# Kernel optimization log

Measured on AMD Instinct MI355X. Metric: run time of the kernel, lower is better.

The kernel has to match this reference:

```python
import jax, jax.numpy as jnp
import numpy as np

B, S, E, H = 4, 1024, 512, 8
DK = E // H


def setup_inputs() -> dict:
    key = jax.random.key(0)
    ks = jax.random.split(key, 16)
    s = 1.0 / np.sqrt(E)
    inp = {
        "query": jax.random.normal(ks[0], (B, S, E), dtype=jnp.float32),
        "key": jax.random.normal(ks[1], (B, S, E), dtype=jnp.float32),
        "value": jax.random.normal(ks[2], (B, S, E), dtype=jnp.float32),
        "dist_conv": jax.random.uniform(ks[3], (B, S, S), dtype=jnp.float32),
        "mask": jax.random.randint(ks[4], (B, S, S), 0, 2, dtype=jnp.int32),
        # four Linear(E, E) layers: q, k, v, out (torch: y = x @ W.T + b)
        "Wq": jax.random.normal(ks[5], (E, E), dtype=jnp.float32) * s,
        "bq": jnp.zeros((E,), dtype=jnp.float32),
        "Wk": jax.random.normal(ks[6], (E, E), dtype=jnp.float32) * s,
        "bk": jnp.zeros((E,), dtype=jnp.float32),
        "Wv": jax.random.normal(ks[7], (E, E), dtype=jnp.float32) * s,
        "bv": jnp.zeros((E,), dtype=jnp.float32),
        "Wo": jax.random.normal(ks[8], (E, E), dtype=jnp.float32) * s,
        "bo": jnp.zeros((E,), dtype=jnp.float32),
        # 1x1 Conv2d(1, H) -> ReLU -> 1x1 Conv2d(H, H)
        "cw1": jax.random.normal(ks[9], (H,), dtype=jnp.float32),  # [out_c] (in_c=1, k=1)
        "cb1": jnp.zeros((H,), dtype=jnp.float32),
        "cw2": jax.random.normal(ks[10], (H, H), dtype=jnp.float32) * (1.0 / np.sqrt(H)),
        "cb2": jnp.zeros((H,), dtype=jnp.float32),
    }
    return inp


def reference(query, key, value, dist_conv, mask, Wq, bq, Wk, bk, Wv, bv, Wo, bo, cw1, cb1, cw2, cb2):
    # projections, split into heads: [B, H, S, DK]
    def proj(x, W, b):
        y = jnp.einsum("bse,fe->bsf", x, W) + b
        return y.reshape(B, S, H, DK).transpose(0, 2, 1, 3)

    q = proj(query, Wq, bq)
    k = proj(key, Wk, bk)
    v = proj(value, Wv, bv)

    # 1x1 conv stack on distance matrix: [B,S,S] -> [B,H,S,S]
    t = jax.nn.relu(dist_conv[:, None] * cw1[None, :, None, None] + cb1[None, :, None, None])
    bias = jnp.einsum("bhij,gh->bgij", t, cw2) + cb2[None, :, None, None]

    scores = jnp.einsum("bhqd,bhkd->bhqk", q, k) / jnp.sqrt(jnp.float32(DK))
    scores = scores * bias
    scores = jnp.where(mask[:, None] == 0, jnp.float32(-1e9), scores)
    p_attn = jax.nn.softmax(scores, axis=-1)

    x = jnp.einsum("bhqk,bhkd->bhqd", p_attn, v)
    x = x.transpose(0, 2, 1, 3).reshape(B, S, E)
    return jnp.einsum("bse,fe->bsf", x, Wo) + bo
```

## Files before the change

kernel.cpp:

```cpp
#include <hip/hip_runtime.h>
#include <hip/hip_bf16.h>
#include <math.h>

#define B_ 4
#define S_ 1024
#define E_ 512
#define H_ 8
#define DK_ 64

typedef short bf16x8 __attribute__((ext_vector_type(8)));
typedef float f32x4 __attribute__((ext_vector_type(4)));

#define MFMA16(a, b, c) __builtin_amdgcn_mfma_f32_16x16x32_bf16((a), (b), (c), 0, 0, 0)
#define cfence() asm volatile("" ::: "memory")

__device__ __forceinline__ void gl_lds16(const void* gptr, void* lptr) {
    __builtin_amdgcn_global_load_lds(
        (const __attribute__((address_space(1))) unsigned int*)gptr,
        (__attribute__((address_space(3))) unsigned int*)lptr,
        16, 0, 0);
}

__device__ __forceinline__ unsigned short bf16_bits(float v) {
    __hip_bfloat16 h = __float2bfloat16(v);
    return *(unsigned short*)&h;
}

__global__ __launch_bounds__(256) void prep(
    const float* __restrict__ q, const float* __restrict__ k, const float* __restrict__ v,
    const float* __restrict__ wq, const float* __restrict__ wk,
    const float* __restrict__ wv, const float* __restrict__ wo,
    const float* __restrict__ dist, const int* __restrict__ mask,
    __hip_bfloat16* qc, __hip_bfloat16* kc, __hip_bfloat16* vc,
    __hip_bfloat16* wqc, __hip_bfloat16* wkc, __hip_bfloat16* wvc, __hip_bfloat16* woc,
    __hip_bfloat16* __restrict__ dM) {
    const int blk = blockIdx.x;
    const int tid = threadIdx.x;
    if (blk >= 3584) {
        const int bi = blk - 3584;
        const int b = bi >> 10, i = bi & 1023;
        const int j0 = tid * 4;
        const size_t dbase = ((size_t)b * 1024 + i) * 1024 + j0;
        float4 d4 = *(const float4*)(dist + dbase);
        int4 m4 = *(const int4*)(mask + dbase);
        float dv[4] = {d4.x, d4.y, d4.z, d4.w};
        int mv[4] = {m4.x, m4.y, m4.z, m4.w};
        union { unsigned short us[4]; uint2 u2; } o;
#pragma unroll
        for (int e = 0; e < 4; ++e) {
            unsigned short u = bf16_bits(dv[e]);
            if (mv[e] == 0) u = 0xFF80u;
            o.us[e] = u;
        }
        *(uint2*)(dM + dbase) = o.u2;
        return;
    }
    const float* src;
    __hip_bfloat16* dst;
    int base;
    if (blk < 1024)      { src = q; dst = qc; base = blk; }
    else if (blk < 2048) { src = k; dst = kc; base = blk - 1024; }
    else if (blk < 3072) { src = v; dst = vc; base = blk - 2048; }
    else {
        const int wz = (blk - 3072) >> 7;
        base = (blk - 3072) & 127;
        switch (wz) {
            case 0: src = wq; dst = wqc; break;
            case 1: src = wk; dst = wkc; break;
            case 2: src = wv; dst = wvc; break;
            default: src = wo; dst = woc; break;
        }
    }
    const int idx = (base * 256 + tid) * 8;
    float4 a = *(const float4*)(src + idx);
    float4 bb = *(const float4*)(src + idx + 4);
    union { __hip_bfloat16 h[8]; uint4 u; } o;
    o.h[0] = __float2bfloat16(a.x);  o.h[1] = __float2bfloat16(a.y);
    o.h[2] = __float2bfloat16(a.z);  o.h[3] = __float2bfloat16(a.w);
    o.h[4] = __float2bfloat16(bb.x); o.h[5] = __float2bfloat16(bb.y);
    o.h[6] = __float2bfloat16(bb.z); o.h[7] = __float2bfloat16(bb.w);
    *(uint4*)(dst + idx) = o.u;
}

template <int NROWS_W, int NT>
__device__ __forceinline__ void gemm_core64(const __hip_bfloat16* A, const __hip_bfloat16* W,
                                            char* sA, char* sW, int m0, int n0,
                                            f32x4 acc[4][NT]) {
    const int t = threadIdx.x;
    const int w = t >> 6, lane = t & 63;
    const int wm = (w >> 1) * 64, wn = (w & 1) * (NT * 16);
    const int g = lane >> 4, ln = lane & 15;
    const int WB = NROWS_W * 128;

    const char* aaddr[4];
    const char* waddr[NROWS_W / 32];
#pragma unroll
    for (int i = 0; i < 4; ++i) {
        int L = (i * 4 + w) * 64 + lane;
        int r = L >> 3, cs = L & 7;
        int c = cs ^ (r & 7);
        aaddr[i] = (const char*)A + (size_t)(m0 + r) * 1024 + c * 16;
    }
#pragma unroll
    for (int i = 0; i < NROWS_W / 32; ++i) {
        int L = (i * 4 + w) * 64 + lane;
        int r = L >> 3, cs = L & 7;
        int c = cs ^ (r & 7);
        waddr[i] = (const char*)W + (size_t)(n0 + r) * 1024 + c * 16;
    }

#pragma unroll
    for (int i = 0; i < 4; ++i) {
        gl_lds16(aaddr[i], sA + (i * 4 + w) * 1024);
        aaddr[i] += 128;
    }
#pragma unroll
    for (int i = 0; i < NROWS_W / 32; ++i) {
        gl_lds16(waddr[i], sW + (i * 4 + w) * 1024);
        waddr[i] += 128;
    }

    for (int kc = 0; kc < 8; ++kc) {
        const int cur = kc & 1;
        __syncthreads();
        if (kc < 7) {
            char* nA = sA + (cur ^ 1) * 16384;
            char* nW = sW + (cur ^ 1) * WB;
#pragma unroll
            for (int i = 0; i < 4; ++i) {
                gl_lds16(aaddr[i], nA + (i * 4 + w) * 1024);
                aaddr[i] += 128;
            }
#pragma unroll
            for (int i = 0; i < NROWS_W / 32; ++i) {
                gl_lds16(waddr[i], nW + (i * 4 + w) * 1024);
                waddr[i] += 128;
            }
        }
        const char* cA = sA + cur * 16384;
        const char* cW = sW + cur * WB;
#pragma unroll
        for (int ks = 0; ks < 2; ++ks) {
            bf16x8 af[4], bf[NT];
#pragma unroll
            for (int mt = 0; mt < 4; ++mt) {
                int m = wm + mt * 16 + ln;
                int c = ks * 4 + g;
                af[mt] = *(const bf16x8*)(cA + m * 128 + (c ^ (m & 7)) * 16);
            }
#pragma unroll
            for (int nt = 0; nt < NT; ++nt) {
                int n = wn + nt * 16 + ln;
                int c = ks * 4 + g;
                bf[nt] = *(const bf16x8*)(cW + n * 128 + (c ^ (n & 7)) * 16);
            }
#pragma unroll
            for (int mt = 0; mt < 4; ++mt)
#pragma unroll
                for (int nt = 0; nt < NT; ++nt)
                    acc[mt][nt] = MFMA16(af[mt], bf[nt], acc[mt][nt]);
        }
    }
}

__global__ __launch_bounds__(256) void proj_gemm(
    const __hip_bfloat16* __restrict__ qc, const __hip_bfloat16* __restrict__ kc,
    const __hip_bfloat16* __restrict__ vc,
    const __hip_bfloat16* __restrict__ wqc, const __hip_bfloat16* __restrict__ wkc,
    const __hip_bfloat16* __restrict__ wvc,
    const float* __restrict__ bq, const float* __restrict__ bk, const float* __restrict__ bv,
    __hip_bfloat16* qbh, __hip_bfloat16* kbh, __hip_bfloat16* vt) {
    __shared__ char smem[65536];
    char* sA = smem;
    char* sW = smem + 32768;
    const int z = blockIdx.z;
    const __hip_bfloat16* A;
    const __hip_bfloat16* W;
    const float* bias;
    __hip_bfloat16* dst;
    float scale;
    if (z == 0)      { A = qc; W = wqc; bias = bq; dst = qbh; scale = 0.125f; }
    else if (z == 1) { A = kc; W = wkc; bias = bk; dst = kbh; scale = 1.f; }
    else             { A = vc; W = wvc; bias = bv; dst = vt;  scale = 1.f; }

    const int m0 = blockIdx.y * 128, n0 = blockIdx.x * 128;
    f32x4 acc[4][4] = {};
    gemm_core64<128, 4>(A, W, sA, sW, m0, n0, acc);
    __syncthreads();

    const int t = threadIdx.x;
    const int w = t >> 6, lane = t & 63;
    const int wm = (w >> 1) * 64, wn = (w & 1) * 64;
    const int g = lane >> 4, ln = lane & 15;
    const int b = m0 >> 10;
    float bv4[4];
#pragma unroll
    for (int nt = 0; nt < 4; ++nt) bv4[nt] = bias[n0 + wn + nt * 16 + ln];

    __hip_bfloat16* T = (__hip_bfloat16*)smem;
    if (z != 2) {
#pragma unroll
        for (int p = 0; p < 2; ++p) {
            if (wm == p * 64) {
#pragma unroll
                for (int mt = 0; mt < 4; ++mt)
#pragma unroll
                    for (int nt = 0; nt < 4; ++nt)
#pragma unroll
                        for (int r = 0; r < 4; ++r)
                            T[(mt * 16 + g * 4 + r) * 136 + wn + nt * 16 + ln] =
                                __float2bfloat16((acc[mt][nt][r] + bv4[nt]) * scale);
            }
            __syncthreads();
            const int lr = t >> 2, quarter = t & 3;
            const char* srow = (const char*)T + lr * 272 + quarter * 64;
            const int s = (m0 & 1023) + p * 64 + lr;
            const int h = (n0 >> 6) + (quarter >> 1);
            char* gdst = (char*)dst +
                         (((size_t)(b * 8 + h) * 1024 + s) * 64 + (quarter & 1) * 32) * 2;
#pragma unroll
            for (int j = 0; j < 4; ++j)
                *(uint4*)(gdst + j * 16) = *(const uint4*)(srow + j * 16);
            __syncthreads();
        }
    } else {
#pragma unroll
        for (int p = 0; p < 2; ++p) {
            if (wm == p * 64) {
#pragma unroll
                for (int mt = 0; mt < 4; ++mt)
#pragma unroll
                    for (int nt = 0; nt < 4; ++nt)
#pragma unroll
                        for (int r = 0; r < 4; ++r)
                            T[(mt * 16 + g * 4 + r) * 130 + wn + nt * 16 + ln] =
                                __float2bfloat16(acc[mt][nt][r] + bv4[nt]);
            }
            __syncthreads();
            const int c = t >> 1, sel = t & 1;
            union { __hip_bfloat16 h[32]; uint4 u[4]; } P;
#pragma unroll
            for (int i = 0; i < 32; ++i)
                P.h[i] = T[(sel * 32 + i) * 130 + c];
            const int h = (n0 >> 6) + (c >> 6), dk = c & 63;
            char* gdst = (char*)vt +
                         (((size_t)(b * 8 + h) * 64 + dk) * 1024 + (m0 & 1023) + p * 64 + sel * 32) * 2;
#pragma unroll
            for (int j = 0; j < 4; ++j)
                *(uint4*)(gdst + j * 16) = P.u[j];
            __syncthreads();
        }
    }
}

__global__ __launch_bounds__(256) void out_gemm(
    const __hip_bfloat16* __restrict__ X, const __hip_bfloat16* __restrict__ woc,
    const float* __restrict__ bo, float* __restrict__ out) {
    __shared__ char smem[49152];
    char* sA = smem;
    char* sW = smem + 32768;
    const int m0 = blockIdx.y * 128, n0 = blockIdx.x * 64;
    f32x4 acc[4][2] = {};
    gemm_core64<64, 2>(X, woc, sA, sW, m0, n0, acc);

    const int t = threadIdx.x;
    const int w = t >> 6, lane = t & 63;
    const int wm = (w >> 1) * 64, wn = (w & 1) * 32;
    const int g = lane >> 4, ln = lane & 15;
    float bv2[2];
#pragma unroll
    for (int nt = 0; nt < 2; ++nt) bv2[nt] = bo[n0 + wn + nt * 16 + ln];
#pragma unroll
    for (int mt = 0; mt < 4; ++mt)
#pragma unroll
        for (int nt = 0; nt < 2; ++nt)
#pragma unroll
            for (int r = 0; r < 4; ++r) {
                int m = m0 + wm + mt * 16 + g * 4 + r;
                int f = n0 + wn + nt * 16 + ln;
                out[(size_t)m * 512 + f] = acc[mt][nt][r] + bv2[nt];
            }
}

__global__ __launch_bounds__(256) void attn_one(
    const __hip_bfloat16* __restrict__ Qb, const __hip_bfloat16* __restrict__ Kb,
    const __hip_bfloat16* __restrict__ Vt, const __hip_bfloat16* __restrict__ dM,
    const float* __restrict__ cw1, const float* __restrict__ cb1,
    const float* __restrict__ cw2, const float* __restrict__ cb2,
    __hip_bfloat16* __restrict__ X) {
    __shared__ char sK[2][8192];
    __shared__ char sV[2][8192];
    __shared__ __hip_bfloat16 sP[4][16 * 72];

    const int t = threadIdx.x, w = t >> 6, lane = t & 63;
    const int g = lane >> 4, ln = lane & 15;
    const int wg = blockIdx.x;
    const int xcd = wg & 7, sub = wg >> 3;
    const int bh = xcd * 4 + (sub >> 4);
    const int q0 = (sub & 15) * 64;

    char* sp = (char*)sP[w];

    const int gh = bh & 7;
    float Pc = 0.f, Cc = cb2[gh];
#pragma unroll
    for (int h = 0; h < 8; ++h) {
        float w2 = cw2[gh * 8 + h];
        Pc = fmaf(w2, fmaxf(cw1[h], 0.f), Pc);
        Cc = fmaf(w2, fmaxf(cb1[h], 0.f), Cc);
    }
    const float LOG2E = 1.4426950408889634f;
    Pc *= LOG2E; Cc *= LOG2E;

    bf16x8 qf[2];
    {
        const char* qbase = (const char*)Qb + ((size_t)bh * 1024 + q0 + w * 16 + ln) * 128;
        qf[0] = *(const bf16x8*)(qbase + g * 16);
        qf[1] = *(const bf16x8*)(qbase + 64 + g * 16);
    }

    const char* kaddr[2];
    const char* vaddr[2];
#pragma unroll
    for (int i = 0; i < 2; ++i) {
        int L = (i * 4 + w) * 64 + lane;
        int r = L >> 3, cs = L & 7;
        int c = cs ^ (r & 7);
        kaddr[i] = (const char*)Kb + (size_t)bh * 131072 + (size_t)r * 128 + c * 16;
        vaddr[i] = (const char*)Vt + (size_t)bh * 131072 + (size_t)r * 2048 + c * 16;
    }
    const char* daddr = (const char*)dM +
        (((size_t)(bh >> 3) * 1024 + q0 + w * 16 + ln) * 1024 + g * 4) * 2;

    float m_st = -1e30f, l_st = 0.f;
    f32x4 O[4] = {};

#pragma unroll
    for (int i = 0; i < 2; ++i) {
        gl_lds16(kaddr[i], sK[0] + (i * 4 + w) * 1024);
        gl_lds16(vaddr[i], sV[0] + (i * 4 + w) * 1024);
        kaddr[i] += 8192;
        vaddr[i] += 128;
    }
    uint2 dn0 = *(const uint2*)(daddr);
    uint2 dn1 = *(const uint2*)(daddr + 32);
    uint2 dn2 = *(const uint2*)(daddr + 64);
    uint2 dn3 = *(const uint2*)(daddr + 96);
    daddr += 128;

    for (int it = 0; it < 16; ++it) {
        const int cur = it & 1;
        __syncthreads();
        uint2 d0 = dn0, d1 = dn1, d2 = dn2, d3 = dn3;
        if (it < 15) {
#pragma unroll
            for (int i = 0; i < 2; ++i) {
                gl_lds16(kaddr[i], sK[cur ^ 1] + (i * 4 + w) * 1024);
                gl_lds16(vaddr[i], sV[cur ^ 1] + (i * 4 + w) * 1024);
                kaddr[i] += 8192;
                vaddr[i] += 128;
            }
            dn0 = *(const uint2*)(daddr);
            dn1 = *(const uint2*)(daddr + 32);
            dn2 = *(const uint2*)(daddr + 64);
            dn3 = *(const uint2*)(daddr + 96);
            daddr += 128;
        }

        f32x4 scv[4] = {};
#pragma unroll
        for (int tt = 0; tt < 4; ++tt)
#pragma unroll
            for (int ks = 0; ks < 2; ++ks) {
                int key = tt * 16 + ln;
                int cc = ks * 4 + g;
                bf16x8 kf = *(const bf16x8*)(sK[cur] + key * 128 + (cc ^ (key & 7)) * 16);
                scv[tt] = MFMA16(kf, qf[ks], scv[tt]);
            }

        float s2[16];
#pragma unroll
        for (int tt = 0; tt < 4; ++tt) {
            uint2 dd = (tt == 0) ? d0 : (tt == 1) ? d1 : (tt == 2) ? d2 : d3;
            unsigned int bbv[4];
            bbv[0] = dd.x << 16;
            bbv[1] = dd.x & 0xFFFF0000u;
            bbv[2] = dd.y << 16;
            bbv[3] = dd.y & 0xFFFF0000u;
#pragma unroll
            for (int rr = 0; rr < 4; ++rr) {
                float f = fmaf(__uint_as_float(bbv[rr]), Pc, Cc);
                float s = scv[tt][rr] * f;
                s = (bbv[rr] == 0xFF800000u) ? -1e9f : s;
                s2[tt * 4 + rr] = s;
            }
        }
        float t8[8];
#pragma unroll
        for (int j = 0; j < 8; ++j) t8[j] = fmaxf(s2[2 * j], s2[2 * j + 1]);
        float t4a = fmaxf(t8[0], t8[1]), t4b = fmaxf(t8[2], t8[3]);
        float t4c = fmaxf(t8[4], t8[5]), t4d = fmaxf(t8[6], t8[7]);
        float mx = fmaxf(fmaxf(t4a, t4b), fmaxf(t4c, t4d));
        mx = fmaxf(mx, __shfl_xor(mx, 16));
        mx = fmaxf(mx, __shfl_xor(mx, 32));

        const bool full = __any(mx > m_st + 8.f);
        float alpha = 1.f;
        if (full) {
            const float mnew = fmaxf(m_st, mx);
            alpha = __builtin_amdgcn_exp2f(m_st - mnew);
            m_st = mnew;
        }
        float pv16[16];
#pragma unroll
        for (int i = 0; i < 16; ++i) pv16[i] = __builtin_amdgcn_exp2f(s2[i] - m_st);
        float r8[8];
#pragma unroll
        for (int j = 0; j < 8; ++j) r8[j] = pv16[2 * j] + pv16[2 * j + 1];
        float r4a = r8[0] + r8[1], r4b = r8[2] + r8[3];
        float r4c = r8[4] + r8[5], r4d = r8[6] + r8[7];
        float rs = (r4a + r4b) + (r4c + r4d);
        rs += __shfl_xor(rs, 16);
        rs += __shfl_xor(rs, 32);
        l_st = (full ? l_st * alpha : l_st) + rs;

#pragma unroll
        for (int tt = 0; tt < 4; ++tt) {
            union { unsigned short u[4]; uint2 v; } pk;
            pk.u[0] = bf16_bits(pv16[tt * 4 + 0]);
            pk.u[1] = bf16_bits(pv16[tt * 4 + 1]);
            pk.u[2] = bf16_bits(pv16[tt * 4 + 2]);
            pk.u[3] = bf16_bits(pv16[tt * 4 + 3]);
            *(uint2*)(sp + ln * 144 + tt * 32 + g * 8) = pk.v;
        }
        cfence();

        if (full) {
            float al4[4];
#pragma unroll
            for (int rr = 0; rr < 4; ++rr)
                al4[rr] = __shfl(alpha, (lane & 48) + g * 4 + rr);
#pragma unroll
            for (int tt = 0; tt < 4; ++tt)
#pragma unroll
                for (int rr = 0; rr < 4; ++rr) O[tt][rr] *= al4[rr];
        }

#pragma unroll
        for (int ks = 0; ks < 2; ++ks) {
            bf16x8 pf = *(const bf16x8*)(sp + ln * 144 + ks * 64 + g * 16);
#pragma unroll
            for (int tt = 0; tt < 4; ++tt) {
                int dk = tt * 16 + ln;
                int cc = ks * 4 + g;
                bf16x8 vf = *(const bf16x8*)(sV[cur] + dk * 128 + (cc ^ (dk & 7)) * 16);
                O[tt] = MFMA16(pf, vf, O[tt]);
            }
        }
        cfence();
    }

    const float inv = 1.f / l_st;
    float iv4[4];
#pragma unroll
    for (int rr = 0; rr < 4; ++rr)
        iv4[rr] = __shfl(inv, (lane & 48) + g * 4 + rr);
    const int b = bh >> 3, h = bh & 7;
#pragma unroll
    for (int rr = 0; rr < 4; ++rr) {
        const int s = q0 + w * 16 + g * 4 + rr;
        __hip_bfloat16* xrow = X + ((size_t)(b * 1024 + s)) * 512 + h * 64;
#pragma unroll
        for (int tt = 0; tt < 4; ++tt)
            xrow[tt * 16 + ln] = __float2bfloat16(O[tt][rr] * iv4[rr]);
    }
}

extern "C" void kernel_launch(void* const* d_in, const int* in_sizes, int n_in,
                              void* d_out, int out_size, void* d_ws, size_t ws_size,
                              hipStream_t stream) {
    (void)in_sizes; (void)n_in; (void)out_size; (void)ws_size;
    const float* query = (const float*)d_in[0];
    const float* key   = (const float*)d_in[1];
    const float* value = (const float*)d_in[2];
    const float* dist  = (const float*)d_in[3];
    const int*   mask  = (const int*)d_in[4];
    const float* Wq = (const float*)d_in[5];
    const float* bq = (const float*)d_in[6];
    const float* Wk = (const float*)d_in[7];
    const float* bk = (const float*)d_in[8];
    const float* Wv = (const float*)d_in[9];
    const float* bv = (const float*)d_in[10];
    const float* Wo = (const float*)d_in[11];
    const float* bo = (const float*)d_in[12];
    const float* cw1 = (const float*)d_in[13];
    const float* cb1 = (const float*)d_in[14];
    const float* cw2 = (const float*)d_in[15];
    const float* cb2 = (const float*)d_in[16];
    float* out = (float*)d_out;

    char* ws = (char*)d_ws;
    const size_t MB = 1 << 20;
    __hip_bfloat16* qc  = (__hip_bfloat16*)(ws + 0 * MB);
    __hip_bfloat16* kc  = (__hip_bfloat16*)(ws + 4 * MB);
    __hip_bfloat16* vc  = (__hip_bfloat16*)(ws + 8 * MB);
    __hip_bfloat16* wqc = (__hip_bfloat16*)(ws + 12 * MB);
    __hip_bfloat16* wkc = (__hip_bfloat16*)(ws + 12 * MB + 512 * 1024);
    __hip_bfloat16* wvc = (__hip_bfloat16*)(ws + 13 * MB);
    __hip_bfloat16* woc = (__hip_bfloat16*)(ws + 13 * MB + 512 * 1024);
    __hip_bfloat16* qbh = (__hip_bfloat16*)(ws + 14 * MB);
    __hip_bfloat16* kbh = (__hip_bfloat16*)(ws + 18 * MB);
    __hip_bfloat16* vt  = (__hip_bfloat16*)(ws + 22 * MB);
    __hip_bfloat16* x   = (__hip_bfloat16*)(ws + 26 * MB);
    __hip_bfloat16* dMp = (__hip_bfloat16*)(ws + 32 * MB);

    hipLaunchKernelGGL(prep, dim3(7680), dim3(256), 0, stream,
                       query, key, value, Wq, Wk, Wv, Wo, dist, mask,
                       qc, kc, vc, wqc, wkc, wvc, woc, dMp);
    hipLaunchKernelGGL(proj_gemm, dim3(4, 32, 3), dim3(256), 0, stream,
                       qc, kc, vc, wqc, wkc, wvc, bq, bk, bv, qbh, kbh, vt);
    hipLaunchKernelGGL(attn_one, dim3(512), dim3(256), 0, stream,
                       qbh, kbh, vt, dMp, cw1, cb1, cw2, cb2, x);
    hipLaunchKernelGGL(out_gemm, dim3(8, 32), dim3(256), 0, stream,
                       x, woc, bo, out);
}
```

Baseline: 174.3 us.

## Load K/V fragments directly from global into registers, removing LDS staging and barriers

Replaces the double-buffered LDS staging of K and V tiles (with per-iteration block barriers) by per-wave direct global loads into register fragments. The K tile is prefetched one step ahead through ping-pong register arrays, and the loop is unrolled by two. MFMA sections are wrapped in s_setprio, and the launch bounds request two blocks per CU. This removes the __syncthreads and LDS round trips, but each wave now fetches K/V redundantly from cache and the last prefetch reads past the current head's data.

```diff
diff --git a/kernel.cpp b/kernel.cpp
--- a/kernel.cpp
+++ b/kernel.cpp
@@ -282,14 +282,12 @@
             }
 }
 
-__global__ __launch_bounds__(256) void attn_one(
+__global__ __launch_bounds__(256, 2) void attn_one(
     const __hip_bfloat16* __restrict__ Qb, const __hip_bfloat16* __restrict__ Kb,
     const __hip_bfloat16* __restrict__ Vt, const __hip_bfloat16* __restrict__ dM,
     const float* __restrict__ cw1, const float* __restrict__ cb1,
     const float* __restrict__ cw2, const float* __restrict__ cb2,
     __hip_bfloat16* __restrict__ X) {
-    __shared__ char sK[2][8192];
-    __shared__ char sV[2][8192];
     __shared__ __hip_bfloat16 sP[4][16 * 72];
 
     const int t = threadIdx.x, w = t >> 6, lane = t & 63;
@@ -319,146 +317,138 @@
         qf[1] = *(const bf16x8*)(qbase + 64 + g * 16);
     }
 
-    const char* kaddr[2];
-    const char* vaddr[2];
-#pragma unroll
-    for (int i = 0; i < 2; ++i) {
-        int L = (i * 4 + w) * 64 + lane;
-        int r = L >> 3, cs = L & 7;
-        int c = cs ^ (r & 7);
-        kaddr[i] = (const char*)Kb + (size_t)bh * 131072 + (size_t)r * 128 + c * 16;
-        vaddr[i] = (const char*)Vt + (size_t)bh * 131072 + (size_t)r * 2048 + c * 16;
-    }
-    const char* daddr = (const char*)dM +
+    const char* kA = (const char*)Kb + (size_t)bh * 131072 + (size_t)ln * 128 + g * 16;
+    const char* kB = kA + 4096;
+    const char* vp[4];
+#pragma unroll
+    for (int tt = 0; tt < 4; ++tt)
+        vp[tt] = (const char*)Vt + (size_t)bh * 131072 + (size_t)(tt * 16 + ln) * 2048 + g * 16;
+    const char* dp = (const char*)dM +
         (((size_t)(bh >> 3) * 1024 + q0 + w * 16 + ln) * 1024 + g * 4) * 2;
 
     float m_st = -1e30f, l_st = 0.f;
     f32x4 O[4] = {};
 
-#pragma unroll
-    for (int i = 0; i < 2; ++i) {
-        gl_lds16(kaddr[i], sK[0] + (i * 4 + w) * 1024);
-        gl_lds16(vaddr[i], sV[0] + (i * 4 + w) * 1024);
-        kaddr[i] += 8192;
-        vaddr[i] += 128;
-    }
-    uint2 dn0 = *(const uint2*)(daddr);
-    uint2 dn1 = *(const uint2*)(daddr + 32);
-    uint2 dn2 = *(const uint2*)(daddr + 64);
-    uint2 dn3 = *(const uint2*)(daddr + 96);
-    daddr += 128;
-
-    for (int it = 0; it < 16; ++it) {
-        const int cur = it & 1;
-        __syncthreads();
-        uint2 d0 = dn0, d1 = dn1, d2 = dn2, d3 = dn3;
-        if (it < 15) {
-#pragma unroll
-            for (int i = 0; i < 2; ++i) {
-                gl_lds16(kaddr[i], sK[cur ^ 1] + (i * 4 + w) * 1024);
-                gl_lds16(vaddr[i], sV[cur ^ 1] + (i * 4 + w) * 1024);
-                kaddr[i] += 8192;
-                vaddr[i] += 128;
-            }
-            dn0 = *(const uint2*)(daddr);
-            dn1 = *(const uint2*)(daddr + 32);
-            dn2 = *(const uint2*)(daddr + 64);
-            dn3 = *(const uint2*)(daddr + 96);
-            daddr += 128;
-        }
-
-        f32x4 scv[4] = {};
-#pragma unroll
-        for (int tt = 0; tt < 4; ++tt)
-#pragma unroll
-            for (int ks = 0; ks < 2; ++ks) {
-                int key = tt * 16 + ln;
-                int cc = ks * 4 + g;
-                bf16x8 kf = *(const bf16x8*)(sK[cur] + key * 128 + (cc ^ (key & 7)) * 16);
-                scv[tt] = MFMA16(kf, qf[ks], scv[tt]);
-            }
-
-        float s2[16];
-#pragma unroll
-        for (int tt = 0; tt < 4; ++tt) {
-            uint2 dd = (tt == 0) ? d0 : (tt == 1) ? d1 : (tt == 2) ? d2 : d3;
-            unsigned int bbv[4];
-            bbv[0] = dd.x << 16;
-            bbv[1] = dd.x & 0xFFFF0000u;
-            bbv[2] = dd.y << 16;
-            bbv[3] = dd.y & 0xFFFF0000u;
-#pragma unroll
-            for (int rr = 0; rr < 4; ++rr) {
-                float f = fmaf(__uint_as_float(bbv[rr]), Pc, Cc);
-                float s = scv[tt][rr] * f;
-                s = (bbv[rr] == 0xFF800000u) ? -1e9f : s;
-                s2[tt * 4 + rr] = s;
-            }
-        }
-        float t8[8];
-#pragma unroll
-        for (int j = 0; j < 8; ++j) t8[j] = fmaxf(s2[2 * j], s2[2 * j + 1]);
-        float t4a = fmaxf(t8[0], t8[1]), t4b = fmaxf(t8[2], t8[3]);
-        float t4c = fmaxf(t8[4], t8[5]), t4d = fmaxf(t8[6], t8[7]);
-        float mx = fmaxf(fmaxf(t4a, t4b), fmaxf(t4c, t4d));
-        mx = fmaxf(mx, __shfl_xor(mx, 16));
-        mx = fmaxf(mx, __shfl_xor(mx, 32));
-
-        const bool full = __any(mx > m_st + 8.f);
-        float alpha = 1.f;
-        if (full) {
-            const float mnew = fmaxf(m_st, mx);
-            alpha = __builtin_amdgcn_exp2f(m_st - mnew);
-            m_st = mnew;
-        }
-        float pv16[16];
-#pragma unroll
-        for (int i = 0; i < 16; ++i) pv16[i] = __builtin_amdgcn_exp2f(s2[i] - m_st);
-        float r8[8];
-#pragma unroll
-        for (int j = 0; j < 8; ++j) r8[j] = pv16[2 * j] + pv16[2 * j + 1];
-        float r4a = r8[0] + r8[1], r4b = r8[2] + r8[3];
-        float r4c = r8[4] + r8[5], r4d = r8[6] + r8[7];
-        float rs = (r4a + r4b) + (r4c + r4d);
-        rs += __shfl_xor(rs, 16);
-        rs += __shfl_xor(rs, 32);
-        l_st = (full ? l_st * alpha : l_st) + rs;
-
-#pragma unroll
-        for (int tt = 0; tt < 4; ++tt) {
-            union { unsigned short u[4]; uint2 v; } pk;
-            pk.u[0] = bf16_bits(pv16[tt * 4 + 0]);
-            pk.u[1] = bf16_bits(pv16[tt * 4 + 1]);
-            pk.u[2] = bf16_bits(pv16[tt * 4 + 2]);
-            pk.u[3] = bf16_bits(pv16[tt * 4 + 3]);
-            *(uint2*)(sp + ln * 144 + tt * 32 + g * 8) = pk.v;
-        }
-        cfence();
-
-        if (full) {
-            float al4[4];
-#pragma unroll
-            for (int rr = 0; rr < 4; ++rr)
-                al4[rr] = __shfl(alpha, (lane & 48) + g * 4 + rr);
-#pragma unroll
-            for (int tt = 0; tt < 4; ++tt)
-#pragma unroll
-                for (int rr = 0; rr < 4; ++rr) O[tt][rr] *= al4[rr];
-        }
-
-#pragma unroll
-        for (int ks = 0; ks < 2; ++ks) {
-            bf16x8 pf = *(const bf16x8*)(sp + ln * 144 + ks * 64 + g * 16);
-#pragma unroll
-            for (int tt = 0; tt < 4; ++tt) {
-                int dk = tt * 16 + ln;
-                int cc = ks * 4 + g;
-                bf16x8 vf = *(const bf16x8*)(sV[cur] + dk * 128 + (cc ^ (dk & 7)) * 16);
-                O[tt] = MFMA16(pf, vf, O[tt]);
-            }
-        }
-        cfence();
-    }
+    bf16x8 ka[8], kb2[8];
+#pragma unroll
+    for (int i = 0; i < 4; ++i) {
+        ka[i] = *(const bf16x8*)(kA + (i >> 1) * 2048 + (i & 1) * 64);
+        ka[4 + i] = *(const bf16x8*)(kB + (i >> 1) * 2048 + (i & 1) * 64);
+    }
+    kA += 8192; kB += 8192;
+    uint2 dc0 = *(const uint2*)(dp);
+    uint2 dc1 = *(const uint2*)(dp + 32);
+    uint2 dc2 = *(const uint2*)(dp + 64);
+    uint2 dc3 = *(const uint2*)(dp + 96);
+    dp += 128;
+
+#define ATTN_ITER(KUSE, KPRE)                                                   \
+    do {                                                                        \
+                       \
+        bf16x8 vf[8];                                                           \
+        _Pragma("unroll") for (int tt = 0; tt < 4; ++tt) {                      \
+            vf[tt * 2] = *(const bf16x8*)(vp[tt]);                              \
+            vf[tt * 2 + 1] = *(const bf16x8*)(vp[tt] + 64);                     \
+        }                                                                       \
+        _Pragma("unroll") for (int i = 0; i < 4; ++i) {                         \
+            KPRE[i] = *(const bf16x8*)(kA + (i >> 1) * 2048 + (i & 1) * 64);    \
+            KPRE[4 + i] = *(const bf16x8*)(kB + (i >> 1) * 2048 + (i & 1) * 64);\
+        }                                                                       \
+        kA += 8192; kB += 8192;                                                 \
+        uint2 nd0 = *(const uint2*)(dp);                                        \
+        uint2 nd1 = *(const uint2*)(dp + 32);                                   \
+        uint2 nd2 = *(const uint2*)(dp + 64);                                   \
+        uint2 nd3 = *(const uint2*)(dp + 96);                                   \
+        dp += 128;                                                              \
+            \
+        f32x4 scv[4] = {};                                                      \
+        __builtin_amdgcn_s_setprio(1);                                          \
+        _Pragma("unroll") for (int tt = 0; tt < 4; ++tt) {                      \
+            scv[tt] = MFMA16(KUSE[tt * 2], qf[0], scv[tt]);                     \
+            scv[tt] = MFMA16(KUSE[tt * 2 + 1], qf[1], scv[tt]);                 \
+        }                                                                       \
+        __builtin_amdgcn_s_setprio(0);                                          \
+                                    \
+        float s2[16];                                                           \
+        _Pragma("unroll") for (int tt = 0; tt < 4; ++tt) {                      \
+            uint2 dd = (tt == 0) ? dc0 : (tt == 1) ? dc1 : (tt == 2) ? dc2 : dc3;\
+            unsigned int bbv[4];                                                \
+            bbv[0] = dd.x << 16;                                                \
+            bbv[1] = dd.x & 0xFFFF0000u;                                        \
+            bbv[2] = dd.y << 16;                                                \
+            bbv[3] = dd.y & 0xFFFF0000u;                                        \
+            _Pragma("unroll") for (int rr = 0; rr < 4; ++rr) {                  \
+                float f = fmaf(__uint_as_float(bbv[rr]), Pc, Cc);               \
+                float s = scv[tt][rr] * f;                                      \
+                s = (bbv[rr] == 0xFF800000u) ? -1e9f : s;                       \
+                s2[tt * 4 + rr] = s;                                            \
+            }                                                                   \
+        }                                                                       \
+        float m1 = fmaxf(fmaxf(s2[0], s2[1]), s2[2]);                           \
+        float m2 = fmaxf(fmaxf(s2[3], s2[4]), s2[5]);                           \
+        float m3 = fmaxf(fmaxf(s2[6], s2[7]), s2[8]);                           \
+        float m4 = fmaxf(fmaxf(s2[9], s2[10]), s2[11]);                         \
+        float m5 = fmaxf(fmaxf(s2[12], s2[13]), s2[14]);                        \
+        float mx = fmaxf(fmaxf(fmaxf(fmaxf(m1, m2), m3), fmaxf(m4, m5)), s2[15]);\
+        mx = fmaxf(mx, __shfl_xor(mx, 16));                                     \
+        mx = fmaxf(mx, __shfl_xor(mx, 32));                                     \
+        const bool full = __any(mx > m_st + 8.f);                               \
+        float alpha = 1.f;                                                      \
+        if (full) {                                                             \
+            const float mnew = fmaxf(m_st, mx);                                 \
+            alpha = __builtin_amdgcn_exp2f(m_st - mnew);                        \
+            m_st = mnew;                                                        \
+        }                                                                       \
+        float pv16[16];                                                         \
+        _Pragma("unroll") for (int i = 0; i < 16; ++i)                          \
+            pv16[i] = __builtin_amdgcn_exp2f(s2[i] - m_st);                     \
+        float r8[8];                                                            \
+        _Pragma("unroll") for (int j = 0; j < 8; ++j)                           \
+            r8[j] = pv16[2 * j] + pv16[2 * j + 1];                              \
+        float rs = ((r8[0] + r8[1]) + (r8[2] + r8[3])) +                        \
+                   ((r8[4] + r8[5]) + (r8[6] + r8[7]));                         \
+        rs += __shfl_xor(rs, 16);                                               \
+        rs += __shfl_xor(rs, 32);                                               \
+        l_st = (full ? l_st * alpha : l_st) + rs;                               \
+               \
+        _Pragma("unroll") for (int tt = 0; tt < 4; ++tt) {                      \
+            union { unsigned short u[4]; uint2 v; } pk;                         \
+            pk.u[0] = bf16_bits(pv16[tt * 4 + 0]);                              \
+            pk.u[1] = bf16_bits(pv16[tt * 4 + 1]);                              \
+            pk.u[2] = bf16_bits(pv16[tt * 4 + 2]);                              \
+            pk.u[3] = bf16_bits(pv16[tt * 4 + 3]);                              \
+            *(uint2*)(sp + ln * 144 + tt * 32 + g * 8) = pk.v;                  \
+        }                                                                       \
+        cfence();                                                               \
+             \
+        bf16x8 pf[2];                                                           \
+        _Pragma("unroll") for (int ks = 0; ks < 2; ++ks)                        \
+            pf[ks] = *(const bf16x8*)(sp + ln * 144 + ks * 64 + g * 16);        \
+        cfence();                                                               \
+        if (full) {                                                             \
+            float al4[4];                                                       \
+            _Pragma("unroll") for (int rr = 0; rr < 4; ++rr)                    \
+                al4[rr] = __shfl(alpha, (lane & 48) + g * 4 + rr);              \
+            _Pragma("unroll") for (int tt = 0; tt < 4; ++tt)                    \
+                _Pragma("unroll") for (int rr = 0; rr < 4; ++rr)                \
+                    O[tt][rr] *= al4[rr];                                       \
+        }                                                                       \
+                             \
+        __builtin_amdgcn_s_setprio(1);                                          \
+        _Pragma("unroll") for (int tt = 0; tt < 4; ++tt) {                      \
+            O[tt] = MFMA16(pf[0], vf[tt * 2], O[tt]);                           \
+            O[tt] = MFMA16(pf[1], vf[tt * 2 + 1], O[tt]);                       \
+        }                                                                       \
+        __builtin_amdgcn_s_setprio(0);                                          \
+        dc0 = nd0; dc1 = nd1; dc2 = nd2; dc3 = nd3;                             \
+        _Pragma("unroll") for (int tt = 0; tt < 4; ++tt) vp[tt] += 128;         \
+    } while (0)
+
+    for (int ith = 0; ith < 8; ++ith) {
+        ATTN_ITER(ka, kb2);
+        ATTN_ITER(kb2, ka);
+    }
+#undef ATTN_ITER
 
     const float inv = 1.f / l_st;
     float iv4[4];
```

New measurement: 219.3 us. +25.8%, slower.
